# Kernel optimization log

Hardware: AMD Instinct MI355X
Metric: run time of the kernel (lower is better)

Reference implementation:

```python
import jax, jax.numpy as jnp
import numpy as np

PAD_ID = 0    # scibert [PAD]
SEP_ID = 103  # scibert [SEP]
IGNORE = 100


def setup_inputs() -> dict:
    key = jax.random.key(0)
    ks = jax.random.split(key, 8)
    B, S, D, T = 64, 512, 768, 2
    return {
        "sequence_output": jax.random.normal(ks[0], (B, S, D), dtype=jnp.float32),
        "input_ids": jax.random.randint(ks[1], (B, S), 0, 31090, dtype=jnp.int64),
        "labels": jax.random.randint(ks[2], (B, S), 0, 2, dtype=jnp.int64),
        "W": jax.random.normal(ks[3], (T, D), dtype=jnp.float32) * 0.02,
        "b": jax.random.normal(ks[4], (T,), dtype=jnp.float32) * 0.02,
        "start_trans": jax.random.normal(ks[5], (T,), dtype=jnp.float32) * 0.1,
        "end_trans": jax.random.normal(ks[6], (T,), dtype=jnp.float32) * 0.1,
        "trans": jax.random.normal(ks[7], (T, T), dtype=jnp.float32) * 0.1,
    }


def _crf_llh_token_mean(em, tags, start, end, trans):
    # em: [B,S,T], tags: [B,S]; mask=None in torchcrf => all-ones mask.
    B, S, T = em.shape
    # numerator: score of the gold path
    em_tag = jnp.take_along_axis(em, tags[..., None], axis=2)[..., 0]        # [B,S]
    tr_tag = trans[tags[:, :-1], tags[:, 1:]]                                 # [B,S-1]
    score = start[tags[:, 0]] + em_tag.sum(1) + tr_tag.sum(1) + end[tags[:, -1]]
    # denominator: forward algorithm over time (scan over S-1 tiny steps)
    alpha0 = start[None, :] + em[:, 0]                                        # [B,T]
    em_rest = jnp.swapaxes(em[:, 1:], 0, 1)                                   # [S-1,B,T]

    def step(alpha, em_t):
        # alpha[b,i] + trans[i,j] + em_t[b,j] -> logsumexp over i
        nxt = jax.nn.logsumexp(alpha[:, :, None] + trans[None], axis=1) + em_t
        return nxt, None

    alpha, _ = jax.lax.scan(step, alpha0, em_rest)
    logZ = jax.nn.logsumexp(alpha + end[None, :], axis=1)                     # [B]
    llh = score - logZ
    # reduction='token_mean' with all-ones mask -> sum / (B*S)
    return llh.sum() / jnp.float32(B * S)


def _crf_viterbi(em, start, end, trans):
    # em: [B,S,T] -> decoded tags [B,S] int32
    B, S, T = em.shape
    score0 = start[None, :] + em[:, 0]                                        # [B,T]
    em_rest = jnp.swapaxes(em[:, 1:], 0, 1)                                   # [S-1,B,T]

    def vstep(score, em_t):
        cand = score[:, :, None] + trans[None] + em_t[:, None, :]             # [B,T,T]
        return cand.max(axis=1), cand.argmax(axis=1).astype(jnp.int32)

    final, hist = jax.lax.scan(vstep, score0, em_rest)                        # hist [S-1,B,T]
    final = final + end[None, :]
    last = jnp.argmax(final, axis=1).astype(jnp.int32)                        # [B]

    def back(tag, bp_t):
        prev = jnp.take_along_axis(bp_t, tag[:, None], axis=1)[:, 0]
        return prev, prev

    _, prevs = jax.lax.scan(back, last, hist, reverse=True)                   # [S-1,B]
    tags = jnp.concatenate([prevs, last[None, :]], axis=0)                    # [S,B]
    return jnp.swapaxes(tags, 0, 1)                                           # [B,S]


def reference(sequence_output, input_ids, labels, W, b, start_trans, end_trans, trans):
    mask = (input_ids != PAD_ID) & (input_ids != SEP_ID) & (labels != IGNORE)  # [B,S] bool
    seq = sequence_output * mask[..., None].astype(sequence_output.dtype)
    labels_m = labels * mask.astype(labels.dtype)
    # probablities = relu(hidden2tag(seq))
    em = jax.nn.relu(jnp.einsum("bsd,td->bst", seq, W) + b)                    # [B,S,2]
    loss = _crf_llh_token_mean(em, labels_m, start_trans, end_trans, trans)
    target_emissions = _crf_viterbi(em, start_trans, end_trans, trans).astype(jnp.float32)
    return (loss, target_emissions, labels_m, mask)
```

## Files before the change

kernel.cpp:

```cpp
#include <hip/hip_runtime.h>

#define BB 64
#define SS 512
#define DD 768
#define NROWS (BB*SS)
#define NEG (-1e30f)
#define NCH 16
#define CL  32

__global__ __launch_bounds__(256) void k_emissions(
    const float* __restrict__ seq,
    const int*   __restrict__ input_ids,
    const int*   __restrict__ labels,
    const float* __restrict__ W,
    const float* __restrict__ bias,
    float* __restrict__ em_t,
    int*   __restrict__ tags_t,
    float* __restrict__ out)
{
    const int lane = threadIdx.x & 63;
    const int wid  = blockIdx.x * 4 + (threadIdx.x >> 6);
    const int base = wid * 4;

    const float4* W4 = (const float4*)W;
    float4 w0[3], w1[3];
#pragma unroll
    for (int j = 0; j < 3; ++j) {
        w0[j] = W4[j*64 + lane];
        w1[j] = W4[192 + j*64 + lane];
    }
    const float b0 = bias[0], b1 = bias[1];

    const float4* s4 = (const float4*)seq;
    float4 v[4][3];
#pragma unroll
    for (int r = 0; r < 4; ++r)
#pragma unroll
        for (int j = 0; j < 3; ++j)
            v[r][j] = s4[(size_t)(base + r)*192 + j*64 + lane];

    float d0[4], d1[4];
#pragma unroll
    for (int r = 0; r < 4; ++r) {
        float a0 = 0.f, a1 = 0.f;
#pragma unroll
        for (int j = 0; j < 3; ++j) {
            float4 x = v[r][j];
            a0 += x.x*w0[j].x + x.y*w0[j].y + x.z*w0[j].z + x.w*w0[j].w;
            a1 += x.x*w1[j].x + x.y*w1[j].y + x.z*w1[j].z + x.w*w1[j].w;
        }
        d0[r] = a0; d1[r] = a1;
    }
#pragma unroll
    for (int m = 32; m >= 1; m >>= 1) {
#pragma unroll
        for (int r = 0; r < 4; ++r) {
            d0[r] += __shfl_xor(d0[r], m, 64);
            d1[r] += __shfl_xor(d1[r], m, 64);
        }
    }
    if (lane == 0) {
        const int4 idv = *(const int4*)(input_ids + base);
        const int4 lbv = *(const int4*)(labels + base);
        const int ida[4] = {idv.x, idv.y, idv.z, idv.w};
        const int lba[4] = {lbv.x, lbv.y, lbv.z, lbv.w};
#pragma unroll
        for (int r = 0; r < 4; ++r) {
            const int row = base + r;
            const int id = ida[r], lab = lba[r];
            const int msk = (id != 0 && id != 103 && lab != 100) ? 1 : 0;
            const int lm  = lab * msk;
            const float e0 = fmaxf((msk ? d0[r] : 0.f) + b0, 0.f);
            const float e1 = fmaxf((msk ? d1[r] : 0.f) + b1, 0.f);
            const int b_ = row >> 9, s_ = row & 511;
            *(float2*)(em_t + (s_*BB + b_)*2) = make_float2(e0, e1);
            tags_t[s_*BB + b_] = lm;
            out[1 + NROWS   + row] = (float)lm;
            out[1 + 2*NROWS + row] = (float)msk;
        }
    }
}

__device__ __forceinline__ float lse2(float x, float y) {
    float m = fmaxf(x, y);
    float d = fminf(x, y) - m;
    return m + __logf(1.f + __expf(d));
}

#define STEP_LE(e_, g_) do { \
    float Ex = __expf((e_).x), Ey = __expf((e_).y); \
    float B00 = X00*Ex, B10 = X10*Ex, B01 = X01*Ey, B11 = X11*Ey; \
    float n00 = fmaf(p00, B00, p01*B10); \
    float n01 = fmaf(p00, B01, p01*B11); \
    float n10 = fmaf(p10, B00, p11*B10); \
    float n11 = fmaf(p10, B01, p11*B11); \
    p00 = n00; p01 = n01; p10 = n10; p11 = n11; \
    score += (ptag ? ((g_) ? t11 : t10) : ((g_) ? t01 : t00)) \
           + ((g_) ? (e_).y : (e_).x); \
    ptag = (g_); \
} while (0)

#define RENORM() do { \
    float m0 = fmaxf(p00, p01), m1 = fmaxf(p10, p11); \
    float r0 = __builtin_amdgcn_rcpf(m0), r1 = __builtin_amdgcn_rcpf(m1); \
    p00 *= r0; p01 *= r0; p10 *= r1; p11 *= r1; \
    lc0 += __logf(m0); lc1 += __logf(m1); \
} while (0)

#define STEP_VP(e_) do { \
    float n0 = fmaxf(V00 + t00, V01 + t10) + (e_).x; \
    float n1 = fmaxf(V00 + t01, V01 + t11) + (e_).y; \
    float n2 = fmaxf(V10 + t00, V11 + t10) + (e_).x; \
    float n3 = fmaxf(V10 + t01, V11 + t11) + (e_).y; \
    V00 = n0; V01 = n1; V10 = n2; V11 = n3; \
} while (0)

#define STEP_BPF(i_, e_) do { \
    float c00 = v0 + t00, c10 = v1 + t10; \
    float c01 = v0 + t01, c11 = v1 + t11; \
    int bp0 = (c10 > c00); int bp1 = (c11 > c01); \
    v0 = fmaxf(c00, c10) + (e_).x; v1 = fmaxf(c01, c11) + (e_).y; \
    unsigned two = (unsigned)(bp0 | (bp1 << 1)); \
    if ((i_) < 16) w0 |= two << (2*(i_)); else w1 |= two << (2*((i_)-16)); \
    int nF0 = bp0 ? F1 : F0; int nF1 = bp1 ? F1 : F0; \
    F0 = nF0; F1 = nF1; \
} while (0)

__global__ __launch_bounds__(1024) void k_crf(
    const float* __restrict__ em_t,
    const int*   __restrict__ tags_t,
    const float* __restrict__ start,
    const float* __restrict__ endt,
    const float* __restrict__ trans,
    float* __restrict__ out)
{
    __shared__ float4 logP4[NCH][BB];
    __shared__ float  scoreP[NCH][BB];
    __shared__ float4 vitP4[NCH][BB];
    __shared__ float2 vbound[NCH][BB];
    __shared__ unsigned char Fsh[NCH][BB];
    __shared__ int lastSh[BB];
    __shared__ unsigned int tagbits[BB*17];

    const int tid = threadIdx.x;
    const int b   = tid & 63;
    const int c   = tid >> 6;
    const int k0  = c * CL;
    const float t00 = trans[0], t01 = trans[1], t10 = trans[2], t11 = trans[3];
    const float s0 = start[0], s1 = start[1];
    const float en0 = endt[0], en1 = endt[1];
    const float2* em2 = (const float2*)em_t;

    if (blockIdx.x == 0) {
        const float X00 = __expf(t00), X01 = __expf(t01),
                    X10 = __expf(t10), X11 = __expf(t11);
        float2 e[8]; int g[8];
        float p00, p01, p10, p11, lc0 = 0.f, lc1 = 0.f, score;
        int ptag;
#pragma unroll
        for (int i = 0; i < 8; ++i) {
            e[i] = em2[(k0+i)*BB + b];
            g[i] = tags_t[(k0+i)*BB + b];
        }
        if (c == 0) {
            p00 = 1.f; p01 = 0.f; p10 = 0.f; p11 = 1.f;
            score = g[0] ? (s1 + e[0].y) : (s0 + e[0].x);
        } else {
            int pt = tags_t[(k0-1)*BB + b];
            float Ex = __expf(e[0].x), Ey = __expf(e[0].y);
            p00 = X00*Ex; p01 = X01*Ey; p10 = X10*Ex; p11 = X11*Ey;
            score = (pt ? (g[0] ? t11 : t10) : (g[0] ? t01 : t00))
                  + (g[0] ? e[0].y : e[0].x);
        }
        ptag = g[0];
#pragma unroll
        for (int i = 1; i < 8; ++i) STEP_LE(e[i], g[i]);
        RENORM();
#pragma unroll
        for (int j = 1; j < 4; ++j) {
#pragma unroll
            for (int i = 0; i < 8; ++i) {
                e[i] = em2[(k0 + j*8 + i)*BB + b];
                g[i] = tags_t[(k0 + j*8 + i)*BB + b];
            }
#pragma unroll
            for (int i = 0; i < 8; ++i) STEP_LE(e[i], g[i]);
            RENORM();
        }
        float P00L = fmaxf(__logf(p00) + lc0, NEG);
        float P01L = fmaxf(__logf(p01) + lc0, NEG);
        float P10L = fmaxf(__logf(p10) + lc1, NEG);
        float P11L = fmaxf(__logf(p11) + lc1, NEG);
        logP4[c][b] = make_float4(P00L, P01L, P10L, P11L);
        scoreP[c][b] = score;
        __syncthreads();
        if (c == 0) {
            float2 em0v = em2[b];
            float a0 = s0 + em0v.x, a1 = s1 + em0v.y, sc = 0.f;
#pragma unroll
            for (int cc = 0; cc < NCH; ++cc) {
                float4 P = logP4[cc][b];
                float n0 = lse2(a0 + P.x, a1 + P.z);
                float n1 = lse2(a0 + P.y, a1 + P.w);
                a0 = n0; a1 = n1;
                sc += scoreP[cc][b];
            }
            int tagL = tags_t[511*BB + b];
            sc += tagL ? en1 : en0;
            float logZ = lse2(a0 + en0, a1 + en1);
            float llh = sc - logZ;
#pragma unroll
            for (int m = 32; m >= 1; m >>= 1) llh += __shfl_xor(llh, m, 64);
            if (b == 0) out[0] = llh / (float)NROWS;
        }
    } else {
        float2 e[32];
#pragma unroll
        for (int i = 0; i < 32; ++i) e[i] = em2[(k0+i)*BB + b];
        float V00, V01, V10, V11;
        if (c == 0) {
            V00 = 0.f; V01 = NEG; V10 = NEG; V11 = 0.f;
        } else {
            V00 = t00 + e[0].x; V01 = t01 + e[0].y;
            V10 = t10 + e[0].x; V11 = t11 + e[0].y;
        }
#pragma unroll
        for (int i = 1; i < 32; ++i) STEP_VP(e[i]);
        vitP4[c][b] = make_float4(V00, V01, V10, V11);
        __syncthreads();

        if (c == 0) {
            float2 em0v = em2[b];
            float v0 = s0 + em0v.x, v1 = s1 + em0v.y;
            vbound[0][b] = make_float2(v0, v1);
#pragma unroll
            for (int cc = 0; cc < NCH; ++cc) {
                float4 V = vitP4[cc][b];
                float n0 = fmaxf(v0 + V.x, v1 + V.z);
                float n1 = fmaxf(v0 + V.y, v1 + V.w);
                v0 = n0; v1 = n1;
                if (cc < NCH-1) vbound[cc+1][b] = make_float2(v0, v1);
            }
            lastSh[b] = (v1 + en1 > v0 + en0) ? 1 : 0;
        }
        __syncthreads();

        unsigned w0 = 0u, w1 = 0u;
        int F0 = 0, F1 = 1;
        {
            float2 vb = vbound[c][b];
            float v0 = vb.x, v1 = vb.y;
            if (c != 0) STEP_BPF(0, e[0]);
#pragma unroll
            for (int i = 1; i < 32; ++i) STEP_BPF(i, e[i]);
        }
        Fsh[c][b] = (unsigned char)(F0 | (F1 << 1));
        __syncthreads();

        {
            int t = lastSh[b];
            for (int cc = NCH-1; cc > c; --cc)
                t = (Fsh[cc][b] >> t) & 1;
            unsigned word = ((unsigned)t) << 31;
#pragma unroll
            for (int i = 31; i >= 1; --i) {
                unsigned pair = ((i >= 16) ? (w1 >> (2*(i-16)))
                                           : (w0 >> (2*i))) & 3u;
                t = (int)((pair >> t) & 1u);
                word |= ((unsigned)t) << (i - 1);
            }
            tagbits[b*17 + c] = word;
        }
        __syncthreads();

        for (int idx = tid; idx < NROWS; idx += 1024) {
            const int bq = idx >> 9, k = idx & 511;
            unsigned wd = tagbits[bq*17 + (k >> 5)];
            out[1 + idx] = (float)((wd >> (k & 31)) & 1);
        }
    }
}

extern "C" void kernel_launch(void* const* d_in, const int* in_sizes, int n_in,
                              void* d_out, int out_size, void* d_ws, size_t ws_size,
                              hipStream_t stream) {
    const float* seq    = (const float*)d_in[0];
    const int*   ids    = (const int*)  d_in[1];
    const int*   labels = (const int*)  d_in[2];
    const float* W      = (const float*)d_in[3];
    const float* bias   = (const float*)d_in[4];
    const float* start  = (const float*)d_in[5];
    const float* endt   = (const float*)d_in[6];
    const float* trans  = (const float*)d_in[7];
    float* out = (float*)d_out;

    float* em_t   = (float*)d_ws;
    int*   tags_t = (int*)((char*)d_ws + (size_t)65536*sizeof(float));

    k_emissions<<<2048, 256, 0, stream>>>(seq, ids, labels, W, bias, em_t, tags_t, out);
    k_crf<<<2, 1024, 0, stream>>>(em_t, tags_t, start, endt, trans, out);
}
```

Baseline: 173.6 us.

## Split CRF chunk phase into separate multi-block kernel and parallelize emission epilogue

The chunk-local CRF work (forward-algorithm transfer matrices and Viterbi chunk max-plus products) moves out of a 2-block kernel into a new 16-block kernel, one block per time chunk, with the loss and Viterbi paths on separate wavefronts. Results go to global workspace, and a second kernel does the cross-chunk combine and backtrace. The emission epilogue now uses four lanes, one row each, instead of lane 0 handling all four rows. This spreads the serial chunk work over more CUs, at the cost of an extra kernel launch and a global-memory round trip for the intermediates.

New measurement: 172.2 us, median of 2. About the same (-0.8%).

```diff
diff --git a/kernel.cpp b/kernel.cpp
--- a/kernel.cpp
+++ b/kernel.cpp
@@ -59,25 +59,21 @@
             d1[r] += __shfl_xor(d1[r], m, 64);
         }
     }
-    if (lane == 0) {
-        const int4 idv = *(const int4*)(input_ids + base);
-        const int4 lbv = *(const int4*)(labels + base);
-        const int ida[4] = {idv.x, idv.y, idv.z, idv.w};
-        const int lba[4] = {lbv.x, lbv.y, lbv.z, lbv.w};
-#pragma unroll
-        for (int r = 0; r < 4; ++r) {
-            const int row = base + r;
-            const int id = ida[r], lab = lba[r];
-            const int msk = (id != 0 && id != 103 && lab != 100) ? 1 : 0;
-            const int lm  = lab * msk;
-            const float e0 = fmaxf((msk ? d0[r] : 0.f) + b0, 0.f);
-            const float e1 = fmaxf((msk ? d1[r] : 0.f) + b1, 0.f);
-            const int b_ = row >> 9, s_ = row & 511;
-            *(float2*)(em_t + (s_*BB + b_)*2) = make_float2(e0, e1);
-            tags_t[s_*BB + b_] = lm;
-            out[1 + NROWS   + row] = (float)lm;
-            out[1 + 2*NROWS + row] = (float)msk;
-        }
+    if (lane < 4) {
+        const float dd0 = (lane==0) ? d0[0] : (lane==1) ? d0[1] : (lane==2) ? d0[2] : d0[3];
+        const float dd1 = (lane==0) ? d1[0] : (lane==1) ? d1[1] : (lane==2) ? d1[2] : d1[3];
+        const int row = base + lane;
+        const int id  = input_ids[row];
+        const int lab = labels[row];
+        const int msk = (id != 0 && id != 103 && lab != 100) ? 1 : 0;
+        const int lm  = lab * msk;
+        const float e0 = fmaxf((msk ? dd0 : 0.f) + b0, 0.f);
+        const float e1 = fmaxf((msk ? dd1 : 0.f) + b1, 0.f);
+        const int b_ = row >> 9, s_ = row & 511;
+        *(float2*)(em_t + (s_*BB + b_)*2) = make_float2(e0, e1);
+        tags_t[s_*BB + b_] = lm;
+        out[1 + NROWS   + row] = (float)lm;
+        out[1 + 2*NROWS + row] = (float)msk;
     }
 }
 
@@ -126,42 +122,33 @@
     F0 = nF0; F1 = nF1; \
 } while (0)
 
-__global__ __launch_bounds__(1024) void k_crf(
+__global__ __launch_bounds__(128, 1) void k_crf1(
     const float* __restrict__ em_t,
     const int*   __restrict__ tags_t,
     const float* __restrict__ start,
-    const float* __restrict__ endt,
     const float* __restrict__ trans,
-    float* __restrict__ out)
+    float* __restrict__ logP4g,
+    float* __restrict__ scoreg,
+    float* __restrict__ vitP4g)
 {
-    __shared__ float4 logP4[NCH][BB];
-    __shared__ float  scoreP[NCH][BB];
-    __shared__ float4 vitP4[NCH][BB];
-    __shared__ float2 vbound[NCH][BB];
-    __shared__ unsigned char Fsh[NCH][BB];
-    __shared__ int lastSh[BB];
-    __shared__ unsigned int tagbits[BB*17];
-
-    const int tid = threadIdx.x;
-    const int b   = tid & 63;
-    const int c   = tid >> 6;
-    const int k0  = c * CL;
+    const int b  = threadIdx.x & 63;
+    const int c  = blockIdx.x;
+    const int k0 = c * CL;
     const float t00 = trans[0], t01 = trans[1], t10 = trans[2], t11 = trans[3];
-    const float s0 = start[0], s1 = start[1];
-    const float en0 = endt[0], en1 = endt[1];
     const float2* em2 = (const float2*)em_t;
 
-    if (blockIdx.x == 0) {
+    if (threadIdx.x < 64) {
+        const float s0 = start[0], s1 = start[1];
         const float X00 = __expf(t00), X01 = __expf(t01),
                     X10 = __expf(t10), X11 = __expf(t11);
-        float2 e[8]; int g[8];
+        float2 e[32]; int g[32];
+#pragma unroll
+        for (int i = 0; i < 32; ++i) {
+            e[i] = em2[(k0+i)*BB + b];
+            g[i] = tags_t[(k0+i)*BB + b];
+        }
         float p00, p01, p10, p11, lc0 = 0.f, lc1 = 0.f, score;
         int ptag;
-#pragma unroll
-        for (int i = 0; i < 8; ++i) {
-            e[i] = em2[(k0+i)*BB + b];
-            g[i] = tags_t[(k0+i)*BB + b];
-        }
         if (c == 0) {
             p00 = 1.f; p01 = 0.f; p10 = 0.f; p11 = 1.f;
             score = g[0] ? (s1 + e[0].y) : (s0 + e[0].x);
@@ -174,45 +161,16 @@
         }
         ptag = g[0];
 #pragma unroll
-        for (int i = 1; i < 8; ++i) STEP_LE(e[i], g[i]);
-        RENORM();
-#pragma unroll
-        for (int j = 1; j < 4; ++j) {
-#pragma unroll
-            for (int i = 0; i < 8; ++i) {
-                e[i] = em2[(k0 + j*8 + i)*BB + b];
-                g[i] = tags_t[(k0 + j*8 + i)*BB + b];
-            }
-#pragma unroll
-            for (int i = 0; i < 8; ++i) STEP_LE(e[i], g[i]);
-            RENORM();
-        }
-        float P00L = fmaxf(__logf(p00) + lc0, NEG);
-        float P01L = fmaxf(__logf(p01) + lc0, NEG);
-        float P10L = fmaxf(__logf(p10) + lc1, NEG);
-        float P11L = fmaxf(__logf(p11) + lc1, NEG);
-        logP4[c][b] = make_float4(P00L, P01L, P10L, P11L);
-        scoreP[c][b] = score;
-        __syncthreads();
-        if (c == 0) {
-            float2 em0v = em2[b];
-            float a0 = s0 + em0v.x, a1 = s1 + em0v.y, sc = 0.f;
-#pragma unroll
-            for (int cc = 0; cc < NCH; ++cc) {
-                float4 P = logP4[cc][b];
-                float n0 = lse2(a0 + P.x, a1 + P.z);
-                float n1 = lse2(a0 + P.y, a1 + P.w);
-                a0 = n0; a1 = n1;
-                sc += scoreP[cc][b];
-            }
-            int tagL = tags_t[511*BB + b];
-            sc += tagL ? en1 : en0;
-            float logZ = lse2(a0 + en0, a1 + en1);
-            float llh = sc - logZ;
-#pragma unroll
-            for (int m = 32; m >= 1; m >>= 1) llh += __shfl_xor(llh, m, 64);
-            if (b == 0) out[0] = llh / (float)NROWS;
-        }
+        for (int i = 1; i < 32; ++i) {
+            STEP_LE(e[i], g[i]);
+            if ((i & 7) == 7) RENORM();
+        }
+        float4 P = make_float4(fmaxf(__logf(p00) + lc0, NEG),
+                               fmaxf(__logf(p01) + lc0, NEG),
+                               fmaxf(__logf(p10) + lc1, NEG),
+                               fmaxf(__logf(p11) + lc1, NEG));
+        ((float4*)logP4g)[c*BB + b] = P;
+        scoreg[c*BB + b] = score;
     } else {
         float2 e[32];
 #pragma unroll
@@ -226,16 +184,63 @@
         }
 #pragma unroll
         for (int i = 1; i < 32; ++i) STEP_VP(e[i]);
-        vitP4[c][b] = make_float4(V00, V01, V10, V11);
-        __syncthreads();
-
+        ((float4*)vitP4g)[c*BB + b] = make_float4(V00, V01, V10, V11);
+    }
+}
+
+__global__ __launch_bounds__(1024) void k_crf2(
+    const float* __restrict__ em_t,
+    const int*   __restrict__ tags_t,
+    const float* __restrict__ start,
+    const float* __restrict__ endt,
+    const float* __restrict__ trans,
+    const float* __restrict__ logP4g,
+    const float* __restrict__ scoreg,
+    const float* __restrict__ vitP4g,
+    float* __restrict__ out)
+{
+    __shared__ float2 vbound[NCH][BB];
+    __shared__ unsigned char Fsh[NCH][BB];
+    __shared__ int lastSh[BB];
+    __shared__ unsigned int tagbits[BB*17];
+
+    const int tid = threadIdx.x;
+    const int b   = tid & 63;
+    const int c   = tid >> 6;
+    const int k0  = c * CL;
+    const float t00 = trans[0], t01 = trans[1], t10 = trans[2], t11 = trans[3];
+    const float s0 = start[0], s1 = start[1];
+    const float en0 = endt[0], en1 = endt[1];
+    const float2* em2 = (const float2*)em_t;
+
+    if (blockIdx.x == 0) {
+        if (c == 0) {
+            float2 em0v = em2[b];
+            float a0 = s0 + em0v.x, a1 = s1 + em0v.y, sc = 0.f;
+#pragma unroll
+            for (int cc = 0; cc < NCH; ++cc) {
+                float4 P = ((const float4*)logP4g)[cc*BB + b];
+                float n0 = lse2(a0 + P.x, a1 + P.z);
+                float n1 = lse2(a0 + P.y, a1 + P.w);
+                a0 = n0; a1 = n1;
+                sc += scoreg[cc*BB + b];
+            }
+            int tagL = tags_t[511*BB + b];
+            sc += tagL ? en1 : en0;
+            float logZ = lse2(a0 + en0, a1 + en1);
+            float llh = sc - logZ;
+#pragma unroll
+            for (int m = 32; m >= 1; m >>= 1) llh += __shfl_xor(llh, m, 64);
+            if (b == 0) out[0] = llh / (float)NROWS;
+        }
+    } else {
         if (c == 0) {
             float2 em0v = em2[b];
             float v0 = s0 + em0v.x, v1 = s1 + em0v.y;
             vbound[0][b] = make_float2(v0, v1);
 #pragma unroll
             for (int cc = 0; cc < NCH; ++cc) {
-                float4 V = vitP4[cc][b];
+                float4 V = ((const float4*)vitP4g)[cc*BB + b];
                 float n0 = fmaxf(v0 + V.x, v1 + V.z);
                 float n1 = fmaxf(v0 + V.y, v1 + V.w);
                 v0 = n0; v1 = n1;
@@ -250,9 +255,19 @@
         {
             float2 vb = vbound[c][b];
             float v0 = vb.x, v1 = vb.y;
+            float2 e[8];
+#pragma unroll
+            for (int i = 0; i < 8; ++i) e[i] = em2[(k0+i)*BB + b];
             if (c != 0) STEP_BPF(0, e[0]);
 #pragma unroll
-            for (int i = 1; i < 32; ++i) STEP_BPF(i, e[i]);
+            for (int i = 1; i < 8; ++i) STEP_BPF(i, e[i]);
+#pragma unroll
+            for (int j = 1; j < 4; ++j) {
+#pragma unroll
+                for (int i = 0; i < 8; ++i) e[i] = em2[(k0 + j*8 + i)*BB + b];
+#pragma unroll
+                for (int i = 0; i < 8; ++i) STEP_BPF(j*8 + i, e[i]);
+            }
         }
         Fsh[c][b] = (unsigned char)(F0 | (F1 << 1));
         __syncthreads();
@@ -295,8 +310,13 @@
     float* out = (float*)d_out;
 
     float* em_t   = (float*)d_ws;
-    int*   tags_t = (int*)((char*)d_ws + (size_t)65536*sizeof(float));
+    int*   tags_t = (int*)  ((char*)d_ws + (size_t) 65536*4);
+    float* logP4g = (float*)((char*)d_ws + (size_t) 98304*4);
+    float* scoreg = (float*)((char*)d_ws + (size_t)102400*4);
+    float* vitP4g = (float*)((char*)d_ws + (size_t)103424*4);
 
     k_emissions<<<2048, 256, 0, stream>>>(seq, ids, labels, W, bias, em_t, tags_t, out);
-    k_crf<<<2, 1024, 0, stream>>>(em_t, tags_t, start, endt, trans, out);
-}
+    k_crf1<<<16, 128, 0, stream>>>(em_t, tags_t, start, trans, logP4g, scoreg, vitP4g);
+    k_crf2<<<2, 1024, 0, stream>>>(em_t, tags_t, start, endt, trans,
+                                   logP4g, scoreg, vitP4g, out);
+}
```
